# Kernel optimization log

Hardware: AMD Instinct MI355X
Metric: run time of the kernel (lower is better)

Reference implementation:

```python
import jax, jax.numpy as jnp
import numpy as np

D_MODEL = 1024
N_HEADS = 16
D_K = 64
CHUNK_LEN = 64
B, CHUNKS, NEIGHBORS, NEIGHBOR_LEN = 8, 32, 2, 128
SEQ = CHUNKS * CHUNK_LEN  # 2048
LN_EPS = 1e-5


def setup_inputs() -> dict:
    key = jax.random.key(0)
    ks = jax.random.split(key, 8)
    s = 0.02
    return {
        "h": jax.random.normal(ks[0], (B, SEQ, D_MODEL), dtype=jnp.float32),
        "e": jax.random.normal(ks[1], (B, CHUNKS, NEIGHBORS, NEIGHBOR_LEN, D_MODEL), dtype=jnp.float32),
        "Wq": jax.random.normal(ks[2], (D_MODEL, N_HEADS * D_K), dtype=jnp.float32) * s,
        "bq": jnp.zeros((N_HEADS * D_K,), dtype=jnp.float32),
        "Wk": jax.random.normal(ks[3], (D_MODEL, N_HEADS * D_K), dtype=jnp.float32) * s,
        "bk": jnp.zeros((N_HEADS * D_K,), dtype=jnp.float32),
        "Wv": jax.random.normal(ks[4], (D_MODEL, N_HEADS * D_K), dtype=jnp.float32) * s,
        "bv": jnp.zeros((N_HEADS * D_K,), dtype=jnp.float32),
        "gamma": jnp.ones((D_MODEL,), dtype=jnp.float32),
        "beta": jnp.zeros((D_MODEL,), dtype=jnp.float32),
        "Wo": jax.random.normal(ks[5], (N_HEADS * D_K, D_MODEL), dtype=jnp.float32) * s,
        "bo": jnp.zeros((D_MODEL,), dtype=jnp.float32),
    }


def _layer_norm(x, gamma, beta):
    mu = jnp.mean(x, axis=-1, keepdims=True)
    var = jnp.mean(jnp.square(x - mu), axis=-1, keepdims=True)
    return (x - mu) * jax.lax.rsqrt(var + LN_EPS) * gamma + beta


def reference(h, e, Wq, bq, Wk, bk, Wv, bv, gamma, beta, Wo, bo):
    batch, chunks, neighbors, neighbor_len, d_model = e.shape
    seq = h.shape[1]
    scale = 1.0 / np.sqrt(D_K)
    h_res = h

    # shift so each chunk attends only to completed retrieval chunks
    x = h[:, CHUNK_LEN - 1:]                      # [b, seq-(cl-1), d]
    x = _layer_norm(x, gamma, beta)
    pad = chunks * CHUNK_LEN - x.shape[1]
    x = jnp.pad(x, ((0, 0), (0, pad), (0, 0)))    # [b, chunks*cl, d]
    x = x.reshape(batch, chunks, CHUNK_LEN, d_model)

    q = (x @ Wq + bq).reshape(batch, chunks, CHUNK_LEN, N_HEADS, D_K)
    k = (e @ Wk + bk).reshape(batch, chunks, neighbors, neighbor_len, N_HEADS, D_K)
    v = (e @ Wv + bv).reshape(batch, chunks, neighbors, neighbor_len, N_HEADS, D_K)

    attn = jnp.einsum('bcihd,bcnjhd->bchinj', q, k) * scale   # [b,c,h,i,n,j]
    a_shape = attn.shape
    attn = jax.nn.softmax(attn.reshape(*a_shape[:4], -1), axis=-1).reshape(a_shape)

    o = jnp.einsum('bchinj,bcnjhd->bcihd', attn, v)           # [b,c,i,h,d]
    o = o.reshape(batch, chunks * CHUNK_LEN, N_HEADS * D_K)
    o = o @ Wo + bo
    # undo the shift: left-pad by chunk_len-1, truncate to seq
    o = jnp.pad(o, ((0, 0), (CHUNK_LEN - 1, 0), (0, 0)))[:, :seq]
    return o + h_res
```

## Files before the change

### kernel.cpp

```cpp
#include <hip/hip_runtime.h>
#include <hip/hip_bf16.h>

typedef __attribute__((ext_vector_type(8))) short bf16x8;
typedef __attribute__((ext_vector_type(4))) float f32x4;
typedef __attribute__((ext_vector_type(8))) unsigned short u16x8;

static __device__ __forceinline__ unsigned short f2bf(float f) {
  unsigned int u = __builtin_bit_cast(unsigned int, f);
  u += 0x7fffu + ((u >> 16) & 1u);
  return (unsigned short)(u >> 16);
}
static __device__ __forceinline__ unsigned int pk2(float lo, float hi) {
  return (unsigned int)f2bf(lo) | ((unsigned int)f2bf(hi) << 16);
}
static __device__ __forceinline__ void gload_lds16(const void* g, void* l) {
  __builtin_amdgcn_global_load_lds(
      (__attribute__((address_space(1))) void*)(g),
      (__attribute__((address_space(3))) void*)(l), 16, 0, 0);
}

__global__ __launch_bounds__(256) void cvt_bf16(const float* __restrict__ in,
                                                unsigned short* __restrict__ out,
                                                long n8) {
  const long stride = (long)gridDim.x * 256;
  for (long i = (long)blockIdx.x * 256 + threadIdx.x; i < n8; i += stride) {
    const float4 a = ((const float4*)in)[2 * i];
    const float4 b = ((const float4*)in)[2 * i + 1];
    uint4 w;
    w.x = pk2(a.x, a.y);
    w.y = pk2(a.z, a.w);
    w.z = pk2(b.x, b.y);
    w.w = pk2(b.z, b.w);
    ((uint4*)out)[i] = w;
  }
}

__global__ __launch_bounds__(256) void transpose_w(const float* __restrict__ W,
                                                   unsigned short* __restrict__ WT) {
  __shared__ float tile[64][65];
  const int bx = blockIdx.x;
  const int by = blockIdx.y;
  const int t = threadIdx.x;
  const int rr = t >> 6;
  const int cc = t & 63;
#pragma unroll
  for (int i = 0; i < 16; ++i) {
    int r = i * 4 + rr;
    tile[r][cc] = W[(size_t)(by * 64 + r) * 1024 + bx * 64 + cc];
  }
  __syncthreads();
#pragma unroll
  for (int i = 0; i < 16; ++i) {
    int n = i * 4 + rr;
    WT[(size_t)(bx * 64 + n) * 1024 + by * 64 + cc] = f2bf(tile[cc][n]);
  }
}

__global__ __launch_bounds__(256) void ln_kernel(const float* __restrict__ H,
                                                 const float* __restrict__ gamma,
                                                 const float* __restrict__ beta,
                                                 unsigned short* __restrict__ X) {
  const int row = blockIdx.x;
  const int b = row >> 11;
  const int t = row & 2047;
  const int tid = threadIdx.x;
  uint2* xo = (uint2*)(X + (size_t)row * 1024);
  if (t >= 1985) {
    uint2 z;
    z.x = 0;
    z.y = 0;
    xo[tid] = z;
    return;
  }
  const float4* hp = (const float4*)(H + (size_t)(b * 2048 + t + 63) * 1024);
  float4 v = hp[tid];
  float s = v.x + v.y + v.z + v.w;
  float q = v.x * v.x + v.y * v.y + v.z * v.z + v.w * v.w;
#pragma unroll
  for (int off = 32; off > 0; off >>= 1) {
    s += __shfl_down(s, off);
    q += __shfl_down(q, off);
  }
  __shared__ float red[8];
  const int lane = tid & 63, wid = tid >> 6;
  if (lane == 0) {
    red[wid] = s;
    red[4 + wid] = q;
  }
  __syncthreads();
  s = red[0] + red[1] + red[2] + red[3];
  q = red[4] + red[5] + red[6] + red[7];
  const float mu = s * (1.0f / 1024.0f);
  const float var = q * (1.0f / 1024.0f) - mu * mu;
  const float rs = rsqrtf(var + 1e-5f);
  const float4 g = ((const float4*)gamma)[tid];
  const float4 bb = ((const float4*)beta)[tid];
  uint2 w;
  w.x = pk2((v.x - mu) * rs * g.x + bb.x, (v.y - mu) * rs * g.y + bb.y);
  w.y = pk2((v.z - mu) * rs * g.z + bb.z, (v.w - mu) * rs * g.w + bb.w);
  xo[tid] = w;
}

__global__ __launch_bounds__(256) void fill_head(const float* __restrict__ H,
                                                 float* __restrict__ OUT) {
  const int idx = blockIdx.x * 256 + threadIdx.x;
  const int b = idx / 16128;
  const int rem = idx - b * 16128;
  const size_t off = (size_t)b * 524288 + rem;
  ((float4*)OUT)[off] = ((const float4*)H)[off];
}

#define MIDBAR()                                           \
  {                                                        \
    __builtin_amdgcn_s_barrier();                          \
    asm volatile("s_waitcnt lgkmcnt(0)" ::: "memory");     \
  }
#define ENDBAR() __builtin_amdgcn_s_barrier()
#define VMW2() asm volatile("s_waitcnt vmcnt(2)" ::: "memory")

#define LDA_(mh, buf)                                                                   \
  {                                                                                     \
    const char* base_ = (const char*)&lds[buf][wm][0];                                  \
    _Pragma("unroll") for (int mi = 0; mi < 4; ++mi) {                                  \
      const int r_ = (mh) * 64 + mi * 16 + lrow;                                        \
      af[mi][0] = *(const bf16x8*)(base_ + r_ * 128 + (((0 + lk) ^ (r_ & 7)) * 16));    \
      af[mi][1] = *(const bf16x8*)(base_ + r_ * 128 + (((4 + lk) ^ (r_ & 7)) * 16));    \
    }                                                                                   \
  }
#define LDB_(nh, buf)                                                                   \
  {                                                                                     \
    const char* base_ = (const char*)&lds[buf][2 + (wn >> 1)][0];                       \
    _Pragma("unroll") for (int ni = 0; ni < 2; ++ni) {                                  \
      const int r_ = (wn & 1) * 64 + (nh) * 32 + ni * 16 + lrow;                        \
      bfr[ni][0] = *(const bf16x8*)(base_ + r_ * 128 + (((0 + lk) ^ (r_ & 7)) * 16));   \
      bfr[ni][1] = *(const bf16x8*)(base_ + r_ * 128 + (((4 + lk) ^ (r_ & 7)) * 16));   \
    }                                                                                   \
  }
#define MMA_(mh, nh)                                                                    \
  {                                                                                     \
    __builtin_amdgcn_s_setprio(1);                                                      \
    _Pragma("unroll") for (int mi = 0; mi < 4; ++mi)                                    \
        _Pragma("unroll") for (int ni = 0; ni < 2; ++ni) {                              \
      acc[(mh) * 4 + mi][(nh) * 2 + ni] = __builtin_amdgcn_mfma_f32_16x16x32_bf16(      \
          af[mi][0], bfr[ni][0], acc[(mh) * 4 + mi][(nh) * 2 + ni], 0, 0, 0);           \
      acc[(mh) * 4 + mi][(nh) * 2 + ni] = __builtin_amdgcn_mfma_f32_16x16x32_bf16(      \
          af[mi][1], bfr[ni][1], acc[(mh) * 4 + mi][(nh) * 2 + ni], 0, 0, 0);           \
    }                                                                                   \
    __builtin_amdgcn_s_setprio(0);                                                      \
  }

template <int MODE>
__global__ __launch_bounds__(512, 2) void gemm256(
    const unsigned short* __restrict__ A, const unsigned short* __restrict__ BT,
    const float* __restrict__ bias1, const float* __restrict__ bias2,
    unsigned short* __restrict__ C1, unsigned short* __restrict__ C2,
    const float* __restrict__ H, float* __restrict__ OUT) {
  __shared__ alignas(16) unsigned short lds[2][4][128 * 64];
  const int tid = threadIdx.x;
  const int lane = tid & 63;
  const int wid = tid >> 6;
  const int wm = wid >> 2, wn = wid & 3;
  const int lrow = lane & 15, lk = lane >> 4;

  const int nx = gridDim.x;
  const int orig = blockIdx.y * nx + blockIdx.x;
  const int cpx = (nx * gridDim.y) >> 3;
  const int swz = (orig & 7) * cpx + (orig >> 3);
  const int m0 = (swz / nx) * 256;
  const int n0 = (swz % nx) * 256;

  f32x4 acc[8][4] = {};
  bf16x8 af[4][2], bfr[2][2];

  auto STAGE = [&](int slot, int kt) {
    const int buf = kt & 1;
    const int kc = kt < 16 ? kt : 15;
    const unsigned short* src = (slot < 2) ? A + (size_t)(m0 + slot * 128) * 1024
                                           : BT + (size_t)(n0 + (slot - 2) * 128) * 1024;
    unsigned short* dst = &lds[buf][slot][0];
#pragma unroll
    for (int l = 0; l < 2; ++l) {
      const int row = l * 64 + wid * 8 + (lane >> 3);
      const int ch = (lane & 7) ^ (row & 7);
      gload_lds16(src + (size_t)row * 1024 + kc * 64 + ch * 8,
                  (char*)dst + (l * 64 + wid * 8) * 128);
    }
  };

  STAGE(0, 0);
  STAGE(1, 0);
  STAGE(2, 0);
  STAGE(3, 0);
  STAGE(0, 1);
  VMW2();
  __builtin_amdgcn_s_barrier();

  for (int it = 0; it < 8; ++it) {
    const int t = 2 * it;
    LDA_(0, 0);
    LDB_(0, 0);
    STAGE(1, t + 1);
    MIDBAR();
    MMA_(0, 0);
    ENDBAR();
    LDB_(1, 0);
    STAGE(2, t + 1);
    MIDBAR();
    MMA_(0, 1);
    ENDBAR();
    LDA_(1, 0);
    STAGE(3, t + 1);
    MIDBAR();
    MMA_(1, 1);
    ENDBAR();
    LDB_(0, 0);
    STAGE(0, t + 2);
    MIDBAR();
    MMA_(1, 0);
    VMW2();
    ENDBAR();
    LDA_(0, 1);
    LDB_(0, 1);
    STAGE(1, t + 2);
    MIDBAR();
    MMA_(0, 0);
    ENDBAR();
    LDB_(1, 1);
    STAGE(2, t + 2);
    MIDBAR();
    MMA_(0, 1);
    ENDBAR();
    LDA_(1, 1);
    STAGE(3, t + 2);
    MIDBAR();
    MMA_(1, 1);
    ENDBAR();
    LDB_(0, 1);
    STAGE(0, t + 3);
    MIDBAR();
    MMA_(1, 0);
    VMW2();
    ENDBAR();
  }

  const int r0 = lane >> 4;
#pragma unroll
  for (int N = 0; N < 4; ++N) {
    const int col = n0 + wn * 64 + N * 16 + lrow;
    float bsv;
    unsigned short* Cp = C1;
    int ccol = col;
    if (MODE == 0) {
      if (col < 1024) {
        bsv = bias1[col];
      } else {
        bsv = bias2[col - 1024];
        Cp = C2;
        ccol = col - 1024;
      }
    } else {
      bsv = bias1[col];
    }
#pragma unroll
    for (int M = 0; M < 8; ++M) {
      const int row = m0 + wm * 128 + M * 16 + r0 * 4;
#pragma unroll
      for (int r = 0; r < 4; ++r) {
        float v = acc[M][N][r] + bsv;
        if (MODE == 0) {
          Cp[(size_t)(row + r) * 1024 + ccol] = f2bf(v);
        } else {
          const int gr = row + r;
          if ((gr & 2047) < 1985) {
            const size_t idx = (size_t)(gr + 63) * 1024 + col;
            OUT[idx] = H[idx] + v;
          }
        }
      }
    }
  }
}

__global__ __launch_bounds__(256) void attn_kernel(
    const unsigned short* __restrict__ Q, const unsigned short* __restrict__ K,
    const unsigned short* __restrict__ V, unsigned short* __restrict__ O) {
  __shared__ alignas(16) unsigned short k_lds[256 * 64];
  __shared__ alignas(16) unsigned short v_t[64 * 256];
  const int bid = blockIdx.x;
  const int h = bid & 15;
  const int bc = bid >> 4;
  const int tid = threadIdx.x;
  const int lane = tid & 63;
  const int wid = tid >> 6;
  const size_t kv0 = (size_t)bc * 256 * 1024 + h * 64;

  bf16x8 qf[2];
  {
    const size_t qrow = (size_t)bc * 64 + wid * 16 + (lane & 15);
    const unsigned short* qp = Q + qrow * 1024 + h * 64 + (lane >> 4) * 8;
    qf[0] = *(const bf16x8*)(qp);
    qf[1] = *(const bf16x8*)(qp + 32);
  }
#pragma unroll
  for (int it = 0; it < 8; ++it) {
    const int j = it * 32 + (tid >> 3);
    const int c = tid & 7;
    const uint4 kv = *(const uint4*)(K + kv0 + (size_t)j * 1024 + c * 8);
    *(uint4*)((char*)k_lds + j * 128 + ((c ^ (j & 7)) * 16)) = kv;
  }
  {
    const int j = (tid >> 1) * 2;
    const int half = tid & 1;
#pragma unroll
    for (int cc2 = 0; cc2 < 4; ++cc2) {
      const int chunk = half * 4 + cc2;
      const int d0 = chunk * 8;
      u16x8 a = *(const u16x8*)(V + kv0 + (size_t)j * 1024 + d0);
      u16x8 b = *(const u16x8*)(V + kv0 + (size_t)(j + 1) * 1024 + d0);
#pragma unroll
      for (int dd = 0; dd < 8; ++dd) {
        const int d = d0 + dd;
        unsigned int p = (unsigned int)a[dd] | ((unsigned int)b[dd] << 16);
        *(unsigned int*)((char*)v_t + d * 512 + (((j >> 3) ^ (d & 7)) * 16) + ((j & 7) * 2)) = p;
      }
    }
  }
  __syncthreads();

  f32x4 accs[16] = {};
#pragma unroll
  for (int jt = 0; jt < 16; ++jt) {
#pragma unroll
    for (int ks = 0; ks < 2; ++ks) {
      const int r = jt * 16 + (lane & 15);
      bf16x8 kf = *(const bf16x8*)((const char*)k_lds + r * 128 +
                                   (((ks * 4 + (lane >> 4)) ^ (r & 7)) * 16));
      accs[jt] = __builtin_amdgcn_mfma_f32_16x16x32_bf16(qf[ks], kf, accs[jt], 0, 0, 0);
    }
  }
  __syncthreads();

  float inv_[4];
#pragma unroll
  for (int r = 0; r < 4; ++r) {
    float m = accs[0][r];
#pragma unroll
    for (int jt = 1; jt < 16; ++jt) m = fmaxf(m, accs[jt][r]);
#pragma unroll
    for (int mk = 1; mk < 16; mk <<= 1) m = fmaxf(m, __shfl_xor(m, mk));
    float s = 0.f;
#pragma unroll
    for (int jt = 0; jt < 16; ++jt) {
      float p = __expf((accs[jt][r] - m) * 0.125f);
      accs[jt][r] = p;
      s += p;
    }
#pragma unroll
    for (int mk = 1; mk < 16; mk <<= 1) s += __shfl_xor(s, mk);
    inv_[r] = 1.0f / s;
  }
  char* pbase = (char*)k_lds + wid * 8192;
  {
    const int jc = lane & 15;
    const int i0 = (lane >> 4) * 4;
#pragma unroll
    for (int jt = 0; jt < 16; ++jt) {
      const int j = jt * 16 + jc;
#pragma unroll
      for (int r = 0; r < 4; ++r) {
        const int i = i0 + r;
        *(unsigned short*)(pbase + i * 512 + (((j >> 3) ^ (i & 7)) * 16) + ((j & 7) * 2)) =
            f2bf(accs[jt][r] * inv_[r]);
      }
    }
  }
  __syncthreads();

  f32x4 acco[4] = {};
#pragma unroll
  for (int jb = 0; jb < 8; ++jb) {
    const int i = lane & 15;
    bf16x8 pf = *(const bf16x8*)(pbase + i * 512 + (((jb * 4 + (lane >> 4)) ^ (i & 7)) * 16));
#pragma unroll
    for (int ni = 0; ni < 4; ++ni) {
      const int d = ni * 16 + (lane & 15);
      bf16x8 vf = *(const bf16x8*)((const char*)v_t + d * 512 +
                                   (((jb * 4 + (lane >> 4)) ^ (d & 7)) * 16));
      acco[ni] = __builtin_amdgcn_mfma_f32_16x16x32_bf16(pf, vf, acco[ni], 0, 0, 0);
    }
  }
  {
    const size_t row0 = (size_t)bc * 64 + wid * 16 + (lane >> 4) * 4;
#pragma unroll
    for (int ni = 0; ni < 4; ++ni) {
      const int col = h * 64 + ni * 16 + (lane & 15);
#pragma unroll
      for (int r = 0; r < 4; ++r) {
        O[(row0 + r) * 1024 + col] = f2bf(acco[ni][r]);
      }
    }
  }
}

extern "C" void kernel_launch(void* const* d_in, const int* in_sizes, int n_in,
                              void* d_out, int out_size, void* d_ws, size_t ws_size,
                              hipStream_t stream) {
  const float* h = (const float*)d_in[0];
  const float* e = (const float*)d_in[1];
  const float* Wq = (const float*)d_in[2];
  const float* bq = (const float*)d_in[3];
  const float* Wk = (const float*)d_in[4];
  const float* bk = (const float*)d_in[5];
  const float* Wv = (const float*)d_in[6];
  const float* bv = (const float*)d_in[7];
  const float* gamma = (const float*)d_in[8];
  const float* beta = (const float*)d_in[9];
  const float* Wo = (const float*)d_in[10];
  const float* bo = (const float*)d_in[11];
  float* out = (float*)d_out;

  char* ws = (char*)d_ws;
  unsigned short* x = (unsigned short*)ws;
  unsigned short* q = (unsigned short*)(ws + (32ull << 20));
  unsigned short* kbuf = (unsigned short*)(ws + (64ull << 20));
  unsigned short* vbuf = (unsigned short*)(ws + (192ull << 20));
  unsigned short* ebf = (unsigned short*)(ws + (320ull << 20));
  unsigned short* wqT = (unsigned short*)(ws + (448ull << 20));
  unsigned short* wkvT = (unsigned short*)(ws + (450ull << 20));
  unsigned short* woT = (unsigned short*)(ws + (454ull << 20));
  unsigned short* o = x;

  dim3 tb(256);
  cvt_bf16<<<2048, tb, 0, stream>>>(e, ebf, 8388608L);
  transpose_w<<<dim3(16, 16), tb, 0, stream>>>(Wq, wqT);
  transpose_w<<<dim3(16, 16), tb, 0, stream>>>(Wk, wkvT);
  transpose_w<<<dim3(16, 16), tb, 0, stream>>>(Wv, wkvT + 1024 * 1024);
  transpose_w<<<dim3(16, 16), tb, 0, stream>>>(Wo, woT);
  ln_kernel<<<16384, tb, 0, stream>>>(h, gamma, beta, x);
  gemm256<0><<<dim3(4, 64), dim3(512), 0, stream>>>(x, wqT, bq, nullptr, q, nullptr,
                                                    nullptr, nullptr);
  gemm256<0><<<dim3(8, 256), dim3(512), 0, stream>>>(ebf, wkvT, bk, bv, kbuf, vbuf,
                                                     nullptr, nullptr);
  attn_kernel<<<4096, tb, 0, stream>>>(q, kbuf, vbuf, o);
  fill_head<<<504, tb, 0, stream>>>(h, out);
  gemm256<1><<<dim3(4, 64), dim3(512), 0, stream>>>(o, woT, bo, nullptr, nullptr, nullptr,
                                                    h, out);
}
```

Before: 621.3 us.

## Rework GEMM barriers, keep both B-fragment halves, stage bf16 epilogue through LDS, swizzle attention blocks

The GEMM main loop replaces the barrier-plus-lgkmcnt wait with a compiler memory fence, barrier and sched_barrier, and keeps both halves of the B fragments in registers so the redundant LDB_(0) reload is dropped. The MODE 0 epilogue now writes accumulators to LDS and emits coalesced 16-byte bf16 stores instead of scattered 2-byte stores. The attention kernel remaps block indices, presumably to spread work across XCDs. Removing the explicit lgkmcnt wait leaves the compiler responsible for the LDS dependencies. The extra fragment registers may hurt occupancy at 512 threads with two blocks per CU.

Result: faster. 569.4 us (-8.4%).

```diff
diff --git a/kernel.cpp b/kernel.cpp
--- a/kernel.cpp
+++ b/kernel.cpp
@@ -110,12 +110,12 @@
   ((float4*)OUT)[off] = ((const float4*)H)[off];
 }
 
-#define MIDBAR()                                           \
-  {                                                        \
-    __builtin_amdgcn_s_barrier();                          \
-    asm volatile("s_waitcnt lgkmcnt(0)" ::: "memory");     \
-  }
-#define ENDBAR() __builtin_amdgcn_s_barrier()
+#define FENCE_BAR()                                  \
+  {                                                  \
+    asm volatile("" ::: "memory");                   \
+    __builtin_amdgcn_s_barrier();                    \
+    __builtin_amdgcn_sched_barrier(0);               \
+  }
 #define VMW2() asm volatile("s_waitcnt vmcnt(2)" ::: "memory")
 
 #define LDA_(mh, buf)                                                                   \
@@ -132,8 +132,10 @@
     const char* base_ = (const char*)&lds[buf][2 + (wn >> 1)][0];                       \
     _Pragma("unroll") for (int ni = 0; ni < 2; ++ni) {                                  \
       const int r_ = (wn & 1) * 64 + (nh) * 32 + ni * 16 + lrow;                        \
-      bfr[ni][0] = *(const bf16x8*)(base_ + r_ * 128 + (((0 + lk) ^ (r_ & 7)) * 16));   \
-      bfr[ni][1] = *(const bf16x8*)(base_ + r_ * 128 + (((4 + lk) ^ (r_ & 7)) * 16));   \
+      bfr[nh][ni][0] =                                                                  \
+          *(const bf16x8*)(base_ + r_ * 128 + (((0 + lk) ^ (r_ & 7)) * 16));            \
+      bfr[nh][ni][1] =                                                                  \
+          *(const bf16x8*)(base_ + r_ * 128 + (((4 + lk) ^ (r_ & 7)) * 16));            \
     }                                                                                   \
   }
 #define MMA_(mh, nh)                                                                    \
@@ -142,9 +144,9 @@
     _Pragma("unroll") for (int mi = 0; mi < 4; ++mi)                                    \
         _Pragma("unroll") for (int ni = 0; ni < 2; ++ni) {                              \
       acc[(mh) * 4 + mi][(nh) * 2 + ni] = __builtin_amdgcn_mfma_f32_16x16x32_bf16(      \
-          af[mi][0], bfr[ni][0], acc[(mh) * 4 + mi][(nh) * 2 + ni], 0, 0, 0);           \
+          af[mi][0], bfr[nh][ni][0], acc[(mh) * 4 + mi][(nh) * 2 + ni], 0, 0, 0);       \
       acc[(mh) * 4 + mi][(nh) * 2 + ni] = __builtin_amdgcn_mfma_f32_16x16x32_bf16(      \
-          af[mi][1], bfr[ni][1], acc[(mh) * 4 + mi][(nh) * 2 + ni], 0, 0, 0);           \
+          af[mi][1], bfr[nh][ni][1], acc[(mh) * 4 + mi][(nh) * 2 + ni], 0, 0, 0);       \
     }                                                                                   \
     __builtin_amdgcn_s_setprio(0);                                                      \
   }
@@ -170,7 +172,7 @@
   const int n0 = (swz % nx) * 256;
 
   f32x4 acc[8][4] = {};
-  bf16x8 af[4][2], bfr[2][2];
+  bf16x8 af[4][2], bfr[2][2][2];
 
   auto STAGE = [&](int slot, int kt) {
     const int buf = kt & 1;
@@ -200,80 +202,106 @@
     LDA_(0, 0);
     LDB_(0, 0);
     STAGE(1, t + 1);
-    MIDBAR();
+    FENCE_BAR();
     MMA_(0, 0);
-    ENDBAR();
+    FENCE_BAR();
     LDB_(1, 0);
     STAGE(2, t + 1);
-    MIDBAR();
+    FENCE_BAR();
     MMA_(0, 1);
-    ENDBAR();
+    FENCE_BAR();
     LDA_(1, 0);
     STAGE(3, t + 1);
-    MIDBAR();
+    FENCE_BAR();
     MMA_(1, 1);
-    ENDBAR();
-    LDB_(0, 0);
+    FENCE_BAR();
     STAGE(0, t + 2);
-    MIDBAR();
+    FENCE_BAR();
     MMA_(1, 0);
     VMW2();
-    ENDBAR();
+    FENCE_BAR();
     LDA_(0, 1);
     LDB_(0, 1);
     STAGE(1, t + 2);
-    MIDBAR();
+    FENCE_BAR();
     MMA_(0, 0);
-    ENDBAR();
+    FENCE_BAR();
     LDB_(1, 1);
     STAGE(2, t + 2);
-    MIDBAR();
+    FENCE_BAR();
     MMA_(0, 1);
-    ENDBAR();
+    FENCE_BAR();
     LDA_(1, 1);
     STAGE(3, t + 2);
-    MIDBAR();
+    FENCE_BAR();
     MMA_(1, 1);
-    ENDBAR();
-    LDB_(0, 1);
+    FENCE_BAR();
     STAGE(0, t + 3);
-    MIDBAR();
+    FENCE_BAR();
     MMA_(1, 0);
     VMW2();
-    ENDBAR();
-  }
-
-  const int r0 = lane >> 4;
-#pragma unroll
-  for (int N = 0; N < 4; ++N) {
-    const int col = n0 + wn * 64 + N * 16 + lrow;
-    float bsv;
-    unsigned short* Cp = C1;
-    int ccol = col;
-    if (MODE == 0) {
-      if (col < 1024) {
-        bsv = bias1[col];
-      } else {
-        bsv = bias2[col - 1024];
-        Cp = C2;
-        ccol = col - 1024;
-      }
-    } else {
-      bsv = bias1[col];
-    }
-#pragma unroll
-    for (int M = 0; M < 8; ++M) {
-      const int row = m0 + wm * 128 + M * 16 + r0 * 4;
-#pragma unroll
-      for (int r = 0; r < 4; ++r) {
-        float v = acc[M][N][r] + bsv;
-        if (MODE == 0) {
-          Cp[(size_t)(row + r) * 1024 + ccol] = f2bf(v);
-        } else {
+    FENCE_BAR();
+  }
+
+  if (MODE == 0) {
+    const float* bsel = (n0 < 1024) ? bias1 : bias2;
+    const int cbase = (n0 < 1024) ? n0 : (n0 - 1024);
+    unsigned short* Cp0 = (n0 < 1024) ? C1 : C2;
+    float bsv[4];
+#pragma unroll
+    for (int N = 0; N < 4; ++N) bsv[N] = bsel[cbase + wn * 64 + N * 16 + lrow];
+    float* arr = (float*)&lds[0][0][0];
+    const int q4 = lane >> 4;
+    __syncthreads();
+#pragma unroll
+    for (int p = 0; p < 4; ++p) {
+      if (wm == (p >> 1)) {
+#pragma unroll
+        for (int mb = 0; mb < 4; ++mb) {
+          const int M = (p & 1) * 4 + mb;
+#pragma unroll
+          for (int N = 0; N < 4; ++N) {
+            const int cl = wn * 64 + N * 16 + lrow;
+#pragma unroll
+            for (int r = 0; r < 4; ++r) {
+              arr[(mb * 16 + q4 * 4 + r) * 260 + cl] = acc[M][N][r] + bsv[N];
+            }
+          }
+        }
+      }
+      __syncthreads();
+#pragma unroll
+      for (int k = 0; k < 4; ++k) {
+        const int chunk = k * 512 + tid;
+        const int row = chunk >> 5;
+        const int c8 = chunk & 31;
+        const float* s = arr + row * 260 + c8 * 8;
+        float4 f0 = *(const float4*)(s);
+        float4 f1 = *(const float4*)(s + 4);
+        uint4 w;
+        w.x = pk2(f0.x, f0.y);
+        w.y = pk2(f0.z, f0.w);
+        w.z = pk2(f1.x, f1.y);
+        w.w = pk2(f1.z, f1.w);
+        *(uint4*)(Cp0 + (size_t)(m0 + p * 64 + row) * 1024 + cbase + c8 * 8) = w;
+      }
+      __syncthreads();
+    }
+  } else {
+    const int r0 = lane >> 4;
+#pragma unroll
+    for (int N = 0; N < 4; ++N) {
+      const int col = n0 + wn * 64 + N * 16 + lrow;
+      const float bsv = bias1[col];
+#pragma unroll
+      for (int M = 0; M < 8; ++M) {
+        const int row = m0 + wm * 128 + M * 16 + r0 * 4;
+#pragma unroll
+        for (int r = 0; r < 4; ++r) {
           const int gr = row + r;
           if ((gr & 2047) < 1985) {
             const size_t idx = (size_t)(gr + 63) * 1024 + col;
-            OUT[idx] = H[idx] + v;
+            OUT[idx] = H[idx] + acc[M][N][r] + bsv;
           }
         }
       }
@@ -286,9 +314,9 @@
     const unsigned short* __restrict__ V, unsigned short* __restrict__ O) {
   __shared__ alignas(16) unsigned short k_lds[256 * 64];
   __shared__ alignas(16) unsigned short v_t[64 * 256];
-  const int bid = blockIdx.x;
-  const int h = bid & 15;
-  const int bc = bid >> 4;
+  const int w = ((blockIdx.x & 7) << 9) | (blockIdx.x >> 3);
+  const int h = w & 15;
+  const int bc = w >> 4;
   const int tid = threadIdx.x;
   const int lane = tid & 63;
   const int wid = tid >> 6;
```
